# Performance work log

Measured on AMD Instinct MI355X. Metric: run time of the kernel, lower is better.

## Reference

```python
import jax, jax.numpy as jnp
import numpy as np

DIM = 128
N_ITER = 8
L_SIZE = 80000
C_SIZE = 120000
N_EDGES = 480000


def _mlp(x, w1, b1, w2, b2):
    # 2-layer MLP with ReLU (satbench_n_mlp_layers=2, activation='relu')
    return jnp.maximum(x @ w1 + b1, 0.0) @ w2 + b2


def _layer_norm(x, g, b, eps=1e-5):
    mu = jnp.mean(x, axis=-1, keepdims=True)
    var = jnp.var(x, axis=-1, keepdims=True)
    return (x - mu) * jax.lax.rsqrt(var + eps) * g + b


def _ln_lstm_cell(x, h, c, wi, wh, g_ih, b_ih, g_hh, b_hh, g_c, b_c):
    # LayerNormBasicLSTMCell: LN on input/hidden gate pre-activations and on new cell state
    gates = _layer_norm(x @ wi, g_ih, b_ih) + _layer_norm(h @ wh, g_hh, b_hh)
    i, f, g, o = jnp.split(gates, 4, axis=1)
    new_c = jax.nn.sigmoid(f) * c + jax.nn.sigmoid(i) * jnp.tanh(g)
    new_h = jax.nn.sigmoid(o) * jnp.tanh(_layer_norm(new_c, g_c, b_c))
    return new_h, new_c


def setup_inputs() -> dict:
    key = jax.random.key(0)
    ks = jax.random.split(key, 24)
    d = DIM
    s1 = 1.0 / np.sqrt(d)
    s2 = 1.0 / np.sqrt(2 * d)
    inp = {
        'l_size': L_SIZE,
        'c_size': C_SIZE,
        'l_edge_index': jax.random.randint(ks[0], (N_EDGES,), 0, L_SIZE),
        'c_edge_index': jax.random.randint(ks[1], (N_EDGES,), 0, C_SIZE),
        'l_emb': jax.random.normal(ks[2], (L_SIZE, d), jnp.float32),
        'c_emb': jax.random.normal(ks[3], (C_SIZE, d), jnp.float32),
        # l2c message MLP
        'l2c_w1': jax.random.normal(ks[4], (d, d), jnp.float32) * s1,
        'l2c_b1': jnp.zeros((d,), jnp.float32),
        'l2c_w2': jax.random.normal(ks[5], (d, d), jnp.float32) * s1,
        'l2c_b2': jnp.zeros((d,), jnp.float32),
        # c2l message MLP
        'c2l_w1': jax.random.normal(ks[6], (d, d), jnp.float32) * s1,
        'c2l_b1': jnp.zeros((d,), jnp.float32),
        'c2l_w2': jax.random.normal(ks[7], (d, d), jnp.float32) * s1,
        'c2l_b2': jnp.zeros((d,), jnp.float32),
        # clause update LSTM (input=d)
        'cu_wi': jax.random.normal(ks[8], (d, 4 * d), jnp.float32) * s1,
        'cu_wh': jax.random.normal(ks[9], (d, 4 * d), jnp.float32) * s1,
        'cu_g_ih': jnp.ones((4 * d,), jnp.float32),
        'cu_b_ih': jnp.zeros((4 * d,), jnp.float32),
        'cu_g_hh': jnp.ones((4 * d,), jnp.float32),
        'cu_b_hh': jnp.zeros((4 * d,), jnp.float32),
        'cu_g_c': jnp.ones((d,), jnp.float32),
        'cu_b_c': jnp.zeros((d,), jnp.float32),
        # literal update LSTM (input=2*d)
        'lu_wi': jax.random.normal(ks[10], (2 * d, 4 * d), jnp.float32) * s2,
        'lu_wh': jax.random.normal(ks[11], (d, 4 * d), jnp.float32) * s1,
        'lu_g_ih': jnp.ones((4 * d,), jnp.float32),
        'lu_b_ih': jnp.zeros((4 * d,), jnp.float32),
        'lu_g_hh': jnp.ones((4 * d,), jnp.float32),
        'lu_b_hh': jnp.zeros((4 * d,), jnp.float32),
        'lu_g_c': jnp.ones((d,), jnp.float32),
        'lu_b_c': jnp.zeros((d,), jnp.float32),
    }
    return inp


def reference(l_size, c_size, l_edge_index, c_edge_index, l_emb, c_emb,
              l2c_w1, l2c_b1, l2c_w2, l2c_b2,
              c2l_w1, c2l_b1, c2l_w2, c2l_b2,
              cu_wi, cu_wh, cu_g_ih, cu_b_ih, cu_g_hh, cu_b_hh, cu_g_c, cu_b_c,
              lu_wi, lu_wh, lu_g_ih, lu_b_ih, lu_g_hh, lu_b_hh, lu_g_c, lu_b_c):
    d = l_emb.shape[1]
    l_state = jnp.zeros((l_size, d), l_emb.dtype)
    c_state = jnp.zeros((c_size, d), c_emb.dtype)
    l_embs = [l_emb]
    c_embs = [c_emb]
    for _ in range(N_ITER):
        # literal -> clause
        l_msg_feat = _mlp(l_emb, l2c_w1, l2c_b1, l2c_w2, l2c_b2)
        l2c_msg = l_msg_feat[l_edge_index]                             # [E, d] gather
        l2c_aggr = jax.ops.segment_sum(l2c_msg, c_edge_index, num_segments=c_size)
        c_emb, c_state = _ln_lstm_cell(l2c_aggr, c_emb, c_state,
                                       cu_wi, cu_wh, cu_g_ih, cu_b_ih,
                                       cu_g_hh, cu_b_hh, cu_g_c, cu_b_c)
        c_embs.append(c_emb)
        # clause -> literal
        c_msg_feat = _mlp(c_emb, c2l_w1, c2l_b1, c2l_w2, c2l_b2)
        c2l_msg = c_msg_feat[c_edge_index]
        c2l_aggr = jax.ops.segment_sum(c2l_msg, l_edge_index, num_segments=l_size)
        # flip pos/neg literal embeddings (l2l message)
        pl, ul = jnp.split(l_emb.reshape(l_size // 2, 2 * d), 2, axis=1)
        l2l_msg = jnp.concatenate([ul, pl], axis=1).reshape(l_size, d)
        l_emb, l_state = _ln_lstm_cell(jnp.concatenate([c2l_aggr, l2l_msg], axis=1),
                                       l_emb, l_state,
                                       lu_wi, lu_wh, lu_g_ih, lu_b_ih,
                                       lu_g_hh, lu_b_hh, lu_g_c, lu_b_c)
        l_embs.append(l_emb)
    return jnp.stack(l_embs), jnp.stack(c_embs)
```

## Files before the change

### kernel.cpp

```cpp
#include <hip/hip_runtime.h>
#include <hip/hip_bf16.h>

#define L_SIZE 80000
#define C_SIZE 120000
#define N_EDGES 480000
#define DIM 128
#define GDIM 512
#define N_ITER 8

typedef __attribute__((ext_vector_type(8))) short short8;
typedef __attribute__((ext_vector_type(4))) float f32x4;

__device__ __forceinline__ ushort f2bf(float f) {
    uint u = __float_as_uint(f);
    u = u + 0x7FFFu + ((u >> 16) & 1u);
    return (ushort)(u >> 16);
}
__device__ __forceinline__ float bf2f(ushort h) {
    return __uint_as_float(((uint)h) << 16);
}
__device__ __forceinline__ float sigmf(float x) { return 1.f / (1.f + __expf(-x)); }
__device__ __forceinline__ float tanh_f(float x) {
    float e = __expf(2.f * x);
    return 1.f - 2.f / (e + 1.f);
}
__device__ __forceinline__ f32x4 fzero4() {
    f32x4 v; v[0] = v[1] = v[2] = v[3] = 0.f; return v;
}

__global__ __launch_bounds__(256) void count_kernel(
    const int* __restrict__ dst, int* __restrict__ counts)
{
    int i = blockIdx.x * 256 + threadIdx.x;
    atomicAdd(&counts[dst[i]], 1);
}

__global__ __launch_bounds__(1024) void scan_kernel(
    const int* __restrict__ counts, int* __restrict__ offsets, int n)
{
    __shared__ int psum[1024];
    const int tid = threadIdx.x;
    const int chunk = (n + 1023) / 1024;
    int lo = tid * chunk, hi = lo + chunk; if (hi > n) hi = n;
    int s = 0;
    for (int i = lo; i < hi; ++i) s += counts[i];
    psum[tid] = s;
    __syncthreads();
    for (int off = 1; off < 1024; off <<= 1) {
        int v = (tid >= off) ? psum[tid - off] : 0;
        __syncthreads();
        psum[tid] += v;
        __syncthreads();
    }
    int run = tid ? psum[tid - 1] : 0;
    for (int i = lo; i < hi; ++i) { offsets[i] = run; run += counts[i]; }
    if (tid == 1023) offsets[n] = run;
}

__global__ __launch_bounds__(256) void fill_kernel(
    const int* __restrict__ src, const int* __restrict__ dst,
    int* __restrict__ cursor, int* __restrict__ srclist)
{
    int i = blockIdx.x * 256 + threadIdx.x;
    int d = dst[i];
    int pos = atomicAdd(&cursor[d], 1);
    srclist[pos] = src[i];
}

__global__ __launch_bounds__(256) void aggregate_kernel(
    const float* __restrict__ msg, const int* __restrict__ offsets,
    const int* __restrict__ srclist, float* __restrict__ aggr, int nrows)
{
    int row = blockIdx.x * 8 + (threadIdx.x >> 5);
    if (row >= nrows) return;
    int d4 = (threadIdx.x & 31) << 2;
    int s = offsets[row], e = offsets[row + 1];
    float4 acc = {0.f, 0.f, 0.f, 0.f};
    for (int p = s; p < e; ++p) {
        int sr = srclist[p];
        float4 v = *(const float4*)(msg + (size_t)sr * DIM + d4);
        acc.x += v.x; acc.y += v.y; acc.z += v.z; acc.w += v.w;
    }
    *(float4*)(aggr + (size_t)row * DIM + d4) = acc;
}

__device__ __forceinline__ void stageA2(const float* __restrict__ src, int rowBase,
                                        int rowXor, ushort* dst, int tid, int nrows)
{
    const int planeB = nrows * 256;
    for (int idx = tid * 8; idx < nrows * 128; idx += 512 * 8) {
        int r = idx >> 7, k8 = idx & 127;
        const float* p = src + (size_t)((rowBase + r) ^ rowXor) * DIM + k8;
        float4 v0 = *(const float4*)p;
        float4 v1 = *(const float4*)(p + 4);
        float f[8] = {v0.x, v0.y, v0.z, v0.w, v1.x, v1.y, v1.z, v1.w};
        short8 hi, lo;
        #pragma unroll
        for (int j = 0; j < 8; ++j) {
            ushort h = f2bf(f[j]);
            hi[j] = (short)h;
            lo[j] = (short)f2bf(f[j] - bf2f(h));
        }
        int boff = r * 256 + ((k8 * 2) ^ ((r & 7) << 4));
        *(short8*)((char*)dst + boff) = hi;
        *(short8*)((char*)dst + planeB + boff) = lo;
    }
}

__device__ __forceinline__ short8 readA(const ushort* As, int mi, int k0, int lane)
{
    int r = mi * 16 + (lane & 15);
    int kb = (k0 * 2 + ((lane >> 4) << 4)) ^ ((r & 7) << 4);
    return *(const short8*)((const char*)As + r * 256 + kb);
}

__device__ __forceinline__ short8 readB(const ushort* P, int ks, int NC, int cc,
                                        int laneOff)
{
    return *(const short8*)((const char*)P + (((size_t)(ks * NC + cc)) << 10) + laneOff);
}

__global__ __launch_bounds__(256) void pack_w2(const float* __restrict__ W,
                                               ushort* __restrict__ Ph,
                                               ushort* __restrict__ Pl, int K, int N)
{
    int NC = N / 16;
    int total = K * N;
    for (int o = blockIdx.x * 256 + threadIdx.x; o < total; o += gridDim.x * 256) {
        int j = o & 7, hi = (o >> 3) & 3, c = (o >> 5) & 15;
        int rest = o >> 9;
        int cc = rest % NC, ks = rest / NC;
        int row = ks * 32 + hi * 8 + j, col = cc * 16 + c;
        float v = W[(size_t)row * N + col];
        ushort h = f2bf(v);
        Ph[o] = h;
        Pl[o] = f2bf(v - bf2f(h));
    }
}

#define MFMA3(acc, ah, al, bh, bl)                                              \
    acc = __builtin_amdgcn_mfma_f32_16x16x32_bf16(ah, bh, acc, 0, 0, 0);        \
    acc = __builtin_amdgcn_mfma_f32_16x16x32_bf16(ah, bl, acc, 0, 0, 0);        \
    acc = __builtin_amdgcn_mfma_f32_16x16x32_bf16(al, bh, acc, 0, 0, 0);

__global__ __launch_bounds__(512) void mlp_kernel(
    const float* __restrict__ A,
    const ushort* __restrict__ w1Ph, const ushort* __restrict__ w1Pl,
    const float* __restrict__ b1,
    const ushort* __restrict__ w2Ph, const ushort* __restrict__ w2Pl,
    const float* __restrict__ b2,
    float* __restrict__ msg)
{
    __shared__ __align__(16) ushort AsIn[2 * 64 * 128];
    __shared__ __align__(16) ushort AsHid[2 * 64 * 128];
    const int tid = threadIdx.x;
    const int wv = tid >> 6, lane = tid & 63;
    const int cl = lane & 15, hi = lane >> 4;
    const int rowBase = blockIdx.x * 64;
    const int laneOff = (cl * 4 + hi) * 16;
    const int col = wv * 16 + cl;

    stageA2(A, rowBase, 0, AsIn, tid, 64);
    float b1c = b1[col], b2c = b2[col];
    __syncthreads();

    f32x4 acc[4];
    #pragma unroll
    for (int mi = 0; mi < 4; ++mi) acc[mi] = fzero4();
    #pragma unroll
    for (int ks = 0; ks < 4; ++ks) {
        short8 bh = readB(w1Ph, ks, 8, wv, laneOff);
        short8 bl = readB(w1Pl, ks, 8, wv, laneOff);
        #pragma unroll
        for (int mi = 0; mi < 4; ++mi) {
            short8 ah = readA(AsIn, mi, ks * 32, lane);
            short8 al = readA(AsIn + 64 * 128, mi, ks * 32, lane);
            MFMA3(acc[mi], ah, al, bh, bl);
        }
    }
    #pragma unroll
    for (int mi = 0; mi < 4; ++mi)
        #pragma unroll
        for (int q = 0; q < 4; ++q) {
            int row = mi * 16 + hi * 4 + q;
            float v = fmaxf(acc[mi][q] + b1c, 0.f);
            ushort h = f2bf(v);
            int boff = row * 256 + ((2 * col) ^ ((row & 7) << 4));
            *(ushort*)((char*)AsHid + boff) = h;
            *(ushort*)((char*)AsHid + 64 * 256 + boff) = f2bf(v - bf2f(h));
        }
    __syncthreads();

    f32x4 acc2[4];
    #pragma unroll
    for (int mi = 0; mi < 4; ++mi) acc2[mi] = fzero4();
    #pragma unroll
    for (int ks = 0; ks < 4; ++ks) {
        short8 bh = readB(w2Ph, ks, 8, wv, laneOff);
        short8 bl = readB(w2Pl, ks, 8, wv, laneOff);
        #pragma unroll
        for (int mi = 0; mi < 4; ++mi) {
            short8 ah = readA(AsHid, mi, ks * 32, lane);
            short8 al = readA(AsHid + 64 * 128, mi, ks * 32, lane);
            MFMA3(acc2[mi], ah, al, bh, bl);
        }
    }
    #pragma unroll
    for (int mi = 0; mi < 4; ++mi)
        #pragma unroll
        for (int q = 0; q < 4; ++q) {
            int row = mi * 16 + hi * 4 + q;
            msg[(size_t)(rowBase + row) * DIM + col] = acc2[mi][q] + b2c;
        }
}

template<int KX>
__global__ __launch_bounds__(512) void lstm_kernel(
    const float* __restrict__ X0, const float* __restrict__ X1, int xor1,
    const float* __restrict__ Hsrc,
    const ushort* __restrict__ wiPh, const ushort* __restrict__ wiPl,
    const ushort* __restrict__ whPh, const ushort* __restrict__ whPl,
    const float* __restrict__ g_ih, const float* __restrict__ b_ih,
    const float* __restrict__ g_hh, const float* __restrict__ b_hh,
    const float* __restrict__ g_c,  const float* __restrict__ b_c,
    float* __restrict__ c_state, float* __restrict__ h_out)
{
    __shared__ __align__(16) ushort AsX0[2 * 32 * 128];
    __shared__ __align__(16) ushort AsX1[KX == 8 ? 2 * 32 * 128 : 8];
    __shared__ __align__(16) ushort AsH [2 * 32 * 128];
    __shared__ float red4[32][8][4];
    __shared__ float lnst[32][4];
    __shared__ float red2[32][8][2];
    __shared__ float lnc[32][2];

    const int tid = threadIdx.x;
    const int wv = tid >> 6, lane = tid & 63;
    const int cl = lane & 15, hi = lane >> 4;
    const int rowBase = blockIdx.x * 32;
    const int laneOff = (cl * 4 + hi) * 16;
    const int d = wv * 16 + cl;

    stageA2(X0, rowBase, 0, AsX0, tid, 32);
    if (KX == 8) stageA2(X1, rowBase, xor1, AsX1, tid, 32);
    stageA2(Hsrc, rowBase, 0, AsH, tid, 32);

    float gih[4], bih[4], ghh[4], bhh[4];
    #pragma unroll
    for (int jb = 0; jb < 4; ++jb) {
        int col = jb * 128 + d;
        gih[jb] = g_ih[col]; bih[jb] = b_ih[col];
        ghh[jb] = g_hh[col]; bhh[jb] = b_hh[col];
    }
    const float gcv = g_c[d], bcv = b_c[d];

    __syncthreads();

    f32x4 xacc[2][4], hacc[2][4];
    #pragma unroll
    for (int mi = 0; mi < 2; ++mi)
        #pragma unroll
        for (int jb = 0; jb < 4; ++jb) { xacc[mi][jb] = fzero4(); hacc[mi][jb] = fzero4(); }

    #pragma unroll
    for (int ks = 0; ks < KX; ++ks) {
        const ushort* AX = (KX == 8 && ks >= 4) ? AsX1 : AsX0;
        int k0 = (ks & 3) * 32;
        short8 axh0 = readA(AX, 0, k0, lane);
        short8 axl0 = readA(AX + 32 * 128, 0, k0, lane);
        short8 axh1 = readA(AX, 1, k0, lane);
        short8 axl1 = readA(AX + 32 * 128, 1, k0, lane);
        #pragma unroll
        for (int jb = 0; jb < 4; ++jb) {
            short8 bh = readB(wiPh, ks, 32, jb * 8 + wv, laneOff);
            short8 bl = readB(wiPl, ks, 32, jb * 8 + wv, laneOff);
            MFMA3(xacc[0][jb], axh0, axl0, bh, bl);
            MFMA3(xacc[1][jb], axh1, axl1, bh, bl);
        }
        if (ks < 4) {
            short8 ahh0 = readA(AsH, 0, k0, lane);
            short8 ahl0 = readA(AsH + 32 * 128, 0, k0, lane);
            short8 ahh1 = readA(AsH, 1, k0, lane);
            short8 ahl1 = readA(AsH + 32 * 128, 1, k0, lane);
            #pragma unroll
            for (int jb = 0; jb < 4; ++jb) {
                short8 bh = readB(whPh, ks, 32, jb * 8 + wv, laneOff);
                short8 bl = readB(whPl, ks, 32, jb * 8 + wv, laneOff);
                MFMA3(hacc[0][jb], ahh0, ahl0, bh, bl);
                MFMA3(hacc[1][jb], ahh1, ahl1, bh, bl);
            }
        }
    }

    #pragma unroll
    for (int mi = 0; mi < 2; ++mi)
        #pragma unroll
        for (int q = 0; q < 4; ++q) {
            float px = 0.f, pqx = 0.f, ph = 0.f, pqh = 0.f;
            #pragma unroll
            for (int jb = 0; jb < 4; ++jb) {
                float v = xacc[mi][jb][q]; px += v; pqx += v * v;
                float u = hacc[mi][jb][q]; ph += u; pqh += u * u;
            }
            #pragma unroll
            for (int m = 1; m < 16; m <<= 1) {
                px += __shfl_xor(px, m); pqx += __shfl_xor(pqx, m);
                ph += __shfl_xor(ph, m); pqh += __shfl_xor(pqh, m);
            }
            if (cl == 0) {
                int row = mi * 16 + hi * 4 + q;
                red4[row][wv][0] = px; red4[row][wv][1] = pqx;
                red4[row][wv][2] = ph; red4[row][wv][3] = pqh;
            }
        }
    __syncthreads();
    if (tid < 32) {
        float sx = 0.f, qx = 0.f, sh = 0.f, qh = 0.f;
        for (int ww = 0; ww < 8; ++ww) {
            sx += red4[tid][ww][0]; qx += red4[tid][ww][1];
            sh += red4[tid][ww][2]; qh += red4[tid][ww][3];
        }
        const float inv = 1.f / 512.f;
        float mux = sx * inv, muh = sh * inv;
        lnst[tid][0] = mux; lnst[tid][1] = rsqrtf(qx * inv - mux * mux + 1e-5f);
        lnst[tid][2] = muh; lnst[tid][3] = rsqrtf(qh * inv - muh * muh + 1e-5f);
    }
    __syncthreads();

    float cn[2][4], og[2][4];
    #pragma unroll
    for (int mi = 0; mi < 2; ++mi)
        #pragma unroll
        for (int q = 0; q < 4; ++q) {
            int row = mi * 16 + hi * 4 + q;
            float mux = lnst[row][0], rx = lnst[row][1];
            float muh = lnst[row][2], rh = lnst[row][3];
            float g4[4];
            #pragma unroll
            for (int jb = 0; jb < 4; ++jb)
                g4[jb] = (xacc[mi][jb][q] - mux) * rx * gih[jb] + bih[jb]
                       + (hacc[mi][jb][q] - muh) * rh * ghh[jb] + bhh[jb];
            float cp = c_state[(size_t)(rowBase + row) * DIM + d];
            float cv = sigmf(g4[1]) * cp + sigmf(g4[0]) * tanh_f(g4[2]);
            cn[mi][q] = cv; og[mi][q] = g4[3];
            float sc = cv, qc = cv * cv;
            #pragma unroll
            for (int m = 1; m < 16; m <<= 1) {
                sc += __shfl_xor(sc, m); qc += __shfl_xor(qc, m);
            }
            if (cl == 0) { red2[row][wv][0] = sc; red2[row][wv][1] = qc; }
        }
    __syncthreads();
    if (tid < 32) {
        float sc = 0.f, qc = 0.f;
        for (int ww = 0; ww < 8; ++ww) { sc += red2[tid][ww][0]; qc += red2[tid][ww][1]; }
        const float inv = 1.f / 128.f;
        float mu = sc * inv;
        lnc[tid][0] = mu; lnc[tid][1] = rsqrtf(qc * inv - mu * mu + 1e-5f);
    }
    __syncthreads();

    #pragma unroll
    for (int mi = 0; mi < 2; ++mi)
        #pragma unroll
        for (int q = 0; q < 4; ++q) {
            int row = mi * 16 + hi * 4 + q;
            size_t go = (size_t)(rowBase + row) * DIM + d;
            float cv = cn[mi][q];
            float hv = sigmf(og[mi][q]) *
                       tanh_f((cv - lnc[row][0]) * lnc[row][1] * gcv + bcv);
            c_state[go] = cv;
            h_out[go] = hv;
        }
}

extern "C" void kernel_launch(void* const* d_in, const int* in_sizes, int n_in,
                              void* d_out, int out_size, void* d_ws, size_t ws_size,
                              hipStream_t stream)
{
    const int*   l_edge  = (const int*)d_in[2];
    const int*   c_edge  = (const int*)d_in[3];
    const float* l_emb0  = (const float*)d_in[4];
    const float* c_emb0  = (const float*)d_in[5];
    const float* l2c_w1  = (const float*)d_in[6];
    const float* l2c_b1  = (const float*)d_in[7];
    const float* l2c_w2  = (const float*)d_in[8];
    const float* l2c_b2  = (const float*)d_in[9];
    const float* c2l_w1  = (const float*)d_in[10];
    const float* c2l_b1  = (const float*)d_in[11];
    const float* c2l_w2  = (const float*)d_in[12];
    const float* c2l_b2  = (const float*)d_in[13];
    const float* cu_wi   = (const float*)d_in[14];
    const float* cu_wh   = (const float*)d_in[15];
    const float* cu_g_ih = (const float*)d_in[16];
    const float* cu_b_ih = (const float*)d_in[17];
    const float* cu_g_hh = (const float*)d_in[18];
    const float* cu_b_hh = (const float*)d_in[19];
    const float* cu_g_c  = (const float*)d_in[20];
    const float* cu_b_c  = (const float*)d_in[21];
    const float* lu_wi   = (const float*)d_in[22];
    const float* lu_wh   = (const float*)d_in[23];
    const float* lu_g_ih = (const float*)d_in[24];
    const float* lu_b_ih = (const float*)d_in[25];
    const float* lu_g_hh = (const float*)d_in[26];
    const float* lu_b_hh = (const float*)d_in[27];
    const float* lu_g_c  = (const float*)d_in[28];
    const float* lu_b_c  = (const float*)d_in[29];

    float* out = (float*)d_out;
    float* l_slab = out;
    float* c_slab = out + (size_t)9 * L_SIZE * DIM;

    char* wp = (char*)d_ws;
    float*  l_state = (float*)wp;  wp += (size_t)L_SIZE * DIM * 4;
    float*  c_state = (float*)wp;  wp += (size_t)C_SIZE * DIM * 4;
    float*  aggr    = (float*)wp;  wp += (size_t)C_SIZE * DIM * 4;
    float*  msg     = (float*)wp;  wp += (size_t)C_SIZE * DIM * 4;
    int* c_off     = (int*)wp; wp += (C_SIZE + 1) * 4;
    int* l_off     = (int*)wp; wp += (L_SIZE + 1) * 4;
    int* cnt       = (int*)wp; wp += C_SIZE * 4;
    int* cursor    = (int*)wp; wp += C_SIZE * 4;
    int* c_srclist = (int*)wp; wp += N_EDGES * 4;
    int* l_srclist = (int*)wp; wp += N_EDGES * 4;
    ushort* l2c_w1Ph = (ushort*)wp; wp += 128 * 128 * 2;
    ushort* l2c_w1Pl = (ushort*)wp; wp += 128 * 128 * 2;
    ushort* l2c_w2Ph = (ushort*)wp; wp += 128 * 128 * 2;
    ushort* l2c_w2Pl = (ushort*)wp; wp += 128 * 128 * 2;
    ushort* c2l_w1Ph = (ushort*)wp; wp += 128 * 128 * 2;
    ushort* c2l_w1Pl = (ushort*)wp; wp += 128 * 128 * 2;
    ushort* c2l_w2Ph = (ushort*)wp; wp += 128 * 128 * 2;
    ushort* c2l_w2Pl = (ushort*)wp; wp += 128 * 128 * 2;
    ushort* cu_wiPh  = (ushort*)wp; wp += 128 * 512 * 2;
    ushort* cu_wiPl  = (ushort*)wp; wp += 128 * 512 * 2;
    ushort* cu_whPh  = (ushort*)wp; wp += 128 * 512 * 2;
    ushort* cu_whPl  = (ushort*)wp; wp += 128 * 512 * 2;
    ushort* lu_wiPh  = (ushort*)wp; wp += 256 * 512 * 2;
    ushort* lu_wiPl  = (ushort*)wp; wp += 256 * 512 * 2;
    ushort* lu_whPh  = (ushort*)wp; wp += 128 * 512 * 2;
    ushort* lu_whPl  = (ushort*)wp; wp += 128 * 512 * 2;

    const int eb = N_EDGES / 256;

    hipMemsetAsync(cnt, 0, C_SIZE * 4, stream);
    count_kernel<<<eb, 256, 0, stream>>>(c_edge, cnt);
    scan_kernel<<<1, 1024, 0, stream>>>(cnt, c_off, C_SIZE);
    hipMemcpyAsync(cursor, c_off, C_SIZE * 4, hipMemcpyDeviceToDevice, stream);
    fill_kernel<<<eb, 256, 0, stream>>>(l_edge, c_edge, cursor, c_srclist);
    hipMemsetAsync(cnt, 0, L_SIZE * 4, stream);
    count_kernel<<<eb, 256, 0, stream>>>(l_edge, cnt);
    scan_kernel<<<1, 1024, 0, stream>>>(cnt, l_off, L_SIZE);
    hipMemcpyAsync(cursor, l_off, L_SIZE * 4, hipMemcpyDeviceToDevice, stream);
    fill_kernel<<<eb, 256, 0, stream>>>(c_edge, l_edge, cursor, l_srclist);

    pack_w2<<<64, 256, 0, stream>>>(l2c_w1, l2c_w1Ph, l2c_w1Pl, 128, 128);
    pack_w2<<<64, 256, 0, stream>>>(l2c_w2, l2c_w2Ph, l2c_w2Pl, 128, 128);
    pack_w2<<<64, 256, 0, stream>>>(c2l_w1, c2l_w1Ph, c2l_w1Pl, 128, 128);
    pack_w2<<<64, 256, 0, stream>>>(c2l_w2, c2l_w2Ph, c2l_w2Pl, 128, 128);
    pack_w2<<<256, 256, 0, stream>>>(cu_wi, cu_wiPh, cu_wiPl, 128, 512);
    pack_w2<<<256, 256, 0, stream>>>(cu_wh, cu_whPh, cu_whPl, 128, 512);
    pack_w2<<<512, 256, 0, stream>>>(lu_wi, lu_wiPh, lu_wiPl, 256, 512);
    pack_w2<<<256, 256, 0, stream>>>(lu_wh, lu_whPh, lu_whPl, 128, 512);

    hipMemcpyAsync(l_slab, l_emb0, (size_t)L_SIZE * DIM * sizeof(float),
                   hipMemcpyDeviceToDevice, stream);
    hipMemcpyAsync(c_slab, c_emb0, (size_t)C_SIZE * DIM * sizeof(float),
                   hipMemcpyDeviceToDevice, stream);
    hipMemsetAsync(l_state, 0, (size_t)L_SIZE * DIM * sizeof(float), stream);
    hipMemsetAsync(c_state, 0, (size_t)C_SIZE * DIM * sizeof(float), stream);

    for (int t = 0; t < N_ITER; ++t) {
        const float* le = l_slab + (size_t)t * L_SIZE * DIM;
        const float* ce = c_slab + (size_t)t * C_SIZE * DIM;
        float* le1 = l_slab + (size_t)(t + 1) * L_SIZE * DIM;
        float* ce1 = c_slab + (size_t)(t + 1) * C_SIZE * DIM;

        mlp_kernel<<<L_SIZE / 64, 512, 0, stream>>>(le, l2c_w1Ph, l2c_w1Pl, l2c_b1,
                                                    l2c_w2Ph, l2c_w2Pl, l2c_b2, msg);
        aggregate_kernel<<<C_SIZE / 8, 256, 0, stream>>>(msg, c_off, c_srclist,
                                                         aggr, C_SIZE);
        lstm_kernel<4><<<C_SIZE / 32, 512, 0, stream>>>(
            aggr, nullptr, 0, ce, cu_wiPh, cu_wiPl, cu_whPh, cu_whPl,
            cu_g_ih, cu_b_ih, cu_g_hh, cu_b_hh, cu_g_c, cu_b_c,
            c_state, ce1);

        mlp_kernel<<<C_SIZE / 64, 512, 0, stream>>>(ce1, c2l_w1Ph, c2l_w1Pl, c2l_b1,
                                                    c2l_w2Ph, c2l_w2Pl, c2l_b2, msg);
        aggregate_kernel<<<L_SIZE / 8, 256, 0, stream>>>(msg, l_off, l_srclist,
                                                         aggr, L_SIZE);
        lstm_kernel<8><<<L_SIZE / 32, 512, 0, stream>>>(
            aggr, le, 1, le, lu_wiPh, lu_wiPl, lu_whPh, lu_whPl,
            lu_g_ih, lu_b_ih, lu_g_hh, lu_b_hh, lu_g_c, lu_b_c,
            l_state, le1);
    }
}
```

Before: 6.142 ms.

## Fuse iteration loop into persistent megakernel with grid barriers and fused aggregation

Replaces the 48 per-iteration kernel launches with one persistent kernel of 256 blocks. Each block loops over tiles of the MLP and LSTM phases, and the phases are separated by a software grid barrier built on an atomic counter. The segment-sum aggregation is folded into the LSTM staging, which drops the separate aggregate kernel and the fp32 aggr round-trip through memory. The cost is that only 256 blocks give lower parallelism and latency hiding, spin-wait barriers sit between phases, and forward progress depends on all 256 blocks being co-resident.

```diff
diff --git a/kernel.cpp b/kernel.cpp
--- a/kernel.cpp
+++ b/kernel.cpp
@@ -7,6 +7,8 @@
 #define DIM 128
 #define GDIM 512
 #define N_ITER 8
+#define NBLK 256
+#define NTHR 512
 
 typedef __attribute__((ext_vector_type(8))) short short8;
 typedef __attribute__((ext_vector_type(4))) float f32x4;
@@ -65,59 +67,6 @@
     int d = dst[i];
     int pos = atomicAdd(&cursor[d], 1);
     srclist[pos] = src[i];
-}
-
-__global__ __launch_bounds__(256) void aggregate_kernel(
-    const float* __restrict__ msg, const int* __restrict__ offsets,
-    const int* __restrict__ srclist, float* __restrict__ aggr, int nrows)
-{
-    int row = blockIdx.x * 8 + (threadIdx.x >> 5);
-    if (row >= nrows) return;
-    int d4 = (threadIdx.x & 31) << 2;
-    int s = offsets[row], e = offsets[row + 1];
-    float4 acc = {0.f, 0.f, 0.f, 0.f};
-    for (int p = s; p < e; ++p) {
-        int sr = srclist[p];
-        float4 v = *(const float4*)(msg + (size_t)sr * DIM + d4);
-        acc.x += v.x; acc.y += v.y; acc.z += v.z; acc.w += v.w;
-    }
-    *(float4*)(aggr + (size_t)row * DIM + d4) = acc;
-}
-
-__device__ __forceinline__ void stageA2(const float* __restrict__ src, int rowBase,
-                                        int rowXor, ushort* dst, int tid, int nrows)
-{
-    const int planeB = nrows * 256;
-    for (int idx = tid * 8; idx < nrows * 128; idx += 512 * 8) {
-        int r = idx >> 7, k8 = idx & 127;
-        const float* p = src + (size_t)((rowBase + r) ^ rowXor) * DIM + k8;
-        float4 v0 = *(const float4*)p;
-        float4 v1 = *(const float4*)(p + 4);
-        float f[8] = {v0.x, v0.y, v0.z, v0.w, v1.x, v1.y, v1.z, v1.w};
-        short8 hi, lo;
-        #pragma unroll
-        for (int j = 0; j < 8; ++j) {
-            ushort h = f2bf(f[j]);
-            hi[j] = (short)h;
-            lo[j] = (short)f2bf(f[j] - bf2f(h));
-        }
-        int boff = r * 256 + ((k8 * 2) ^ ((r & 7) << 4));
-        *(short8*)((char*)dst + boff) = hi;
-        *(short8*)((char*)dst + planeB + boff) = lo;
-    }
-}
-
-__device__ __forceinline__ short8 readA(const ushort* As, int mi, int k0, int lane)
-{
-    int r = mi * 16 + (lane & 15);
-    int kb = (k0 * 2 + ((lane >> 4) << 4)) ^ ((r & 7) << 4);
-    return *(const short8*)((const char*)As + r * 256 + kb);
-}
-
-__device__ __forceinline__ short8 readB(const ushort* P, int ks, int NC, int cc,
-                                        int laneOff)
-{
-    return *(const short8*)((const char*)P + (((size_t)(ks * NC + cc)) << 10) + laneOff);
 }
 
 __global__ __launch_bounds__(256) void pack_w2(const float* __restrict__ W,
@@ -138,29 +87,72 @@
     }
 }
 
+__device__ __forceinline__ void stageA2(const float* __restrict__ src, int rowBase,
+                                        int rowXor, ushort* dst, int tid, int nrows)
+{
+    const int planeB = nrows * 256;
+    for (int idx = tid * 8; idx < nrows * 128; idx += NTHR * 8) {
+        int r = idx >> 7, k8 = idx & 127;
+        const float* p = src + (size_t)((rowBase + r) ^ rowXor) * DIM + k8;
+        float4 v0 = *(const float4*)p;
+        float4 v1 = *(const float4*)(p + 4);
+        float f[8] = {v0.x, v0.y, v0.z, v0.w, v1.x, v1.y, v1.z, v1.w};
+        short8 hi8, lo8;
+        #pragma unroll
+        for (int j = 0; j < 8; ++j) {
+            ushort h = f2bf(f[j]);
+            hi8[j] = (short)h;
+            lo8[j] = (short)f2bf(f[j] - bf2f(h));
+        }
+        int boff = r * 256 + ((k8 * 2) ^ ((r & 7) << 4));
+        *(short8*)((char*)dst + boff) = hi8;
+        *(short8*)((char*)dst + planeB + boff) = lo8;
+    }
+}
+
+__device__ __forceinline__ short8 readA(const ushort* As, int mi, int k0, int lane)
+{
+    int r = mi * 16 + (lane & 15);
+    int kb = (k0 * 2 + ((lane >> 4) << 4)) ^ ((r & 7) << 4);
+    return *(const short8*)((const char*)As + r * 256 + kb);
+}
+
+__device__ __forceinline__ short8 readB(const ushort* P, int ks, int NC, int cc,
+                                        int laneOff)
+{
+    return *(const short8*)((const char*)P + (((size_t)(ks * NC + cc)) << 10) + laneOff);
+}
+
 #define MFMA3(acc, ah, al, bh, bl)                                              \
     acc = __builtin_amdgcn_mfma_f32_16x16x32_bf16(ah, bh, acc, 0, 0, 0);        \
     acc = __builtin_amdgcn_mfma_f32_16x16x32_bf16(ah, bl, acc, 0, 0, 0);        \
     acc = __builtin_amdgcn_mfma_f32_16x16x32_bf16(al, bh, acc, 0, 0, 0);
 
-__global__ __launch_bounds__(512) void mlp_kernel(
+__device__ __forceinline__ void grid_barrier(int* cnt, int target, int tid)
+{
+    __syncthreads();
+    if (tid == 0) {
+        __threadfence();
+        __hip_atomic_fetch_add(cnt, 1, __ATOMIC_ACQ_REL, __HIP_MEMORY_SCOPE_AGENT);
+        while (__hip_atomic_load(cnt, __ATOMIC_ACQUIRE, __HIP_MEMORY_SCOPE_AGENT) < target)
+            __builtin_amdgcn_s_sleep(2);
+        __threadfence();
+    }
+    __syncthreads();
+}
+
+__device__ __forceinline__ void mlp_block(
     const float* __restrict__ A,
     const ushort* __restrict__ w1Ph, const ushort* __restrict__ w1Pl,
     const float* __restrict__ b1,
     const ushort* __restrict__ w2Ph, const ushort* __restrict__ w2Pl,
     const float* __restrict__ b2,
-    float* __restrict__ msg)
-{
-    __shared__ __align__(16) ushort AsIn[2 * 64 * 128];
-    __shared__ __align__(16) ushort AsHid[2 * 64 * 128];
-    const int tid = threadIdx.x;
-    const int wv = tid >> 6, lane = tid & 63;
-    const int cl = lane & 15, hi = lane >> 4;
-    const int rowBase = blockIdx.x * 64;
-    const int laneOff = (cl * 4 + hi) * 16;
+    float* __restrict__ msg, int rowBase,
+    ushort* AsIn, ushort* AsHid,
+    int tid, int wv, int lane, int cl, int hi, int laneOff)
+{
+    stageA2(A, rowBase, 0, AsIn, tid, 64);
     const int col = wv * 16 + cl;
-
-    stageA2(A, rowBase, 0, AsIn, tid, 64);
     float b1c = b1[col], b2c = b2[col];
     __syncthreads();
 
@@ -212,38 +204,53 @@
             int row = mi * 16 + hi * 4 + q;
             msg[(size_t)(rowBase + row) * DIM + col] = acc2[mi][q] + b2c;
         }
+    __syncthreads();
 }
 
 template<int KX>
-__global__ __launch_bounds__(512) void lstm_kernel(
-    const float* __restrict__ X0, const float* __restrict__ X1, int xor1,
-    const float* __restrict__ Hsrc,
+__device__ __forceinline__ void lstm_block(
+    const float* __restrict__ msg, const int* __restrict__ offs,
+    const int* __restrict__ srcl,
+    const float* __restrict__ X1src, const float* __restrict__ Hsrc,
     const ushort* __restrict__ wiPh, const ushort* __restrict__ wiPl,
     const ushort* __restrict__ whPh, const ushort* __restrict__ whPl,
     const float* __restrict__ g_ih, const float* __restrict__ b_ih,
     const float* __restrict__ g_hh, const float* __restrict__ b_hh,
     const float* __restrict__ g_c,  const float* __restrict__ b_c,
-    float* __restrict__ c_state, float* __restrict__ h_out)
-{
-    __shared__ __align__(16) ushort AsX0[2 * 32 * 128];
-    __shared__ __align__(16) ushort AsX1[KX == 8 ? 2 * 32 * 128 : 8];
-    __shared__ __align__(16) ushort AsH [2 * 32 * 128];
-    __shared__ float red4[32][8][4];
-    __shared__ float lnst[32][4];
-    __shared__ float red2[32][8][2];
-    __shared__ float lnc[32][2];
-
-    const int tid = threadIdx.x;
-    const int wv = tid >> 6, lane = tid & 63;
-    const int cl = lane & 15, hi = lane >> 4;
-    const int rowBase = blockIdx.x * 32;
-    const int laneOff = (cl * 4 + hi) * 16;
+    float* __restrict__ c_state, float* __restrict__ h_out, int rowBase,
+    ushort* AsX0, ushort* AsX1, ushort* AsH,
+    float (*red4)[8][4], float (*lnst)[4], float (*red2)[8][2], float (*lnc)[2],
+    int tid, int wv, int lane, int cl, int hi, int laneOff)
+{
+    {
+        int r = tid >> 4;
+        int d8 = (tid & 15) << 3;
+        int row = rowBase + r;
+        int s = offs[row], e = offs[row + 1];
+        float a0=0,a1=0,a2=0,a3=0,a4=0,a5=0,a6=0,a7=0;
+        for (int p = s; p < e; ++p) {
+            const float* mp = msg + (size_t)srcl[p] * DIM + d8;
+            float4 v0 = *(const float4*)mp;
+            float4 v1 = *(const float4*)(mp + 4);
+            a0 += v0.x; a1 += v0.y; a2 += v0.z; a3 += v0.w;
+            a4 += v1.x; a5 += v1.y; a6 += v1.z; a7 += v1.w;
+        }
+        float f[8] = {a0,a1,a2,a3,a4,a5,a6,a7};
+        short8 hi8, lo8;
+        #pragma unroll
+        for (int j = 0; j < 8; ++j) {
+            ushort h = f2bf(f[j]);
+            hi8[j] = (short)h;
+            lo8[j] = (short)f2bf(f[j] - bf2f(h));
+        }
+        int boff = r * 256 + ((d8 * 2) ^ ((r & 7) << 4));
+        *(short8*)((char*)AsX0 + boff) = hi8;
+        *(short8*)((char*)AsX0 + 32 * 256 + boff) = lo8;
+    }
+    stageA2(Hsrc, rowBase, 0, AsH, tid, 32);
+    if (KX == 8) stageA2(X1src, rowBase, 1, AsX1, tid, 32);
+
     const int d = wv * 16 + cl;
-
-    stageA2(X0, rowBase, 0, AsX0, tid, 32);
-    if (KX == 8) stageA2(X1, rowBase, xor1, AsX1, tid, 32);
-    stageA2(Hsrc, rowBase, 0, AsH, tid, 32);
-
     float gih[4], bih[4], ghh[4], bhh[4];
     #pragma unroll
     for (int jb = 0; jb < 4; ++jb) {
@@ -252,7 +259,6 @@
         ghh[jb] = g_hh[col]; bhh[jb] = b_hh[col];
     }
     const float gcv = g_c[d], bcv = b_c[d];
-
     __syncthreads();
 
     f32x4 xacc[2][4], hacc[2][4];
@@ -371,6 +377,84 @@
             c_state[go] = cv;
             h_out[go] = hv;
         }
+    __syncthreads();
+}
+
+__global__ __launch_bounds__(NTHR, 2) void mega_kernel(
+    float* __restrict__ l_slab, float* __restrict__ c_slab,
+    float* __restrict__ l_state, float* __restrict__ c_state,
+    float* __restrict__ msg,
+    const int* __restrict__ c_off, const int* __restrict__ c_srclist,
+    const int* __restrict__ l_off, const int* __restrict__ l_srclist,
+    const ushort* l2c_w1Ph, const ushort* l2c_w1Pl, const float* l2c_b1,
+    const ushort* l2c_w2Ph, const ushort* l2c_w2Pl, const float* l2c_b2,
+    const ushort* c2l_w1Ph, const ushort* c2l_w1Pl, const float* c2l_b1,
+    const ushort* c2l_w2Ph, const ushort* c2l_w2Pl, const float* c2l_b2,
+    const ushort* cu_wiPh, const ushort* cu_wiPl,
+    const ushort* cu_whPh, const ushort* cu_whPl,
+    const float* cu_g_ih, const float* cu_b_ih,
+    const float* cu_g_hh, const float* cu_b_hh,
+    const float* cu_g_c,  const float* cu_b_c,
+    const ushort* lu_wiPh, const ushort* lu_wiPl,
+    const ushort* lu_whPh, const ushort* lu_whPl,
+    const float* lu_g_ih, const float* lu_b_ih,
+    const float* lu_g_hh, const float* lu_b_hh,
+    const float* lu_g_c,  const float* lu_b_c,
+    int* __restrict__ barCnt)
+{
+    __shared__ __align__(16) union ShU {
+        struct { ushort in[2 * 64 * 128]; ushort hid[2 * 64 * 128]; } m;
+        struct {
+            ushort x0[2 * 32 * 128];
+            ushort x1[2 * 32 * 128];
+            ushort h [2 * 32 * 128];
+            float red4[32][8][4];
+            float lnst[32][4];
+            float red2[32][8][2];
+            float lnc[32][2];
+        } s;
+    } sh;
+
+    const int tid = threadIdx.x;
+    const int wv = tid >> 6, lane = tid & 63;
+    const int cl = lane & 15, hi = lane >> 4;
+    const int laneOff = (cl * 4 + hi) * 16;
+    int bar = 0;
+
+    for (int t = 0; t < N_ITER; ++t) {
+        const float* le = l_slab + (size_t)t * L_SIZE * DIM;
+        const float* ce = c_slab + (size_t)t * C_SIZE * DIM;
+        float* le1 = l_slab + (size_t)(t + 1) * L_SIZE * DIM;
+        float* ce1 = c_slab + (size_t)(t + 1) * C_SIZE * DIM;
+
+        for (int tb = blockIdx.x; tb < L_SIZE / 64; tb += NBLK)
+            mlp_block(le, l2c_w1Ph, l2c_w1Pl, l2c_b1, l2c_w2Ph, l2c_w2Pl, l2c_b2,
+                      msg, tb * 64, sh.m.in, sh.m.hid, tid, wv, lane, cl, hi, laneOff);
+        grid_barrier(barCnt, (++bar) * NBLK, tid);
+
+        for (int tb = blockIdx.x; tb < C_SIZE / 32; tb += NBLK)
+            lstm_block<4>(msg, c_off, c_srclist, nullptr, ce,
+                          cu_wiPh, cu_wiPl, cu_whPh, cu_whPl,
+                          cu_g_ih, cu_b_ih, cu_g_hh, cu_b_hh, cu_g_c, cu_b_c,
+                          c_state, ce1, tb * 32,
+                          sh.s.x0, sh.s.x1, sh.s.h, sh.s.red4, sh.s.lnst,
+                          sh.s.red2, sh.s.lnc, tid, wv, lane, cl, hi, laneOff);
+        grid_barrier(barCnt, (++bar) * NBLK, tid);
+
+        for (int tb = blockIdx.x; tb < C_SIZE / 64; tb += NBLK)
+            mlp_block(ce1, c2l_w1Ph, c2l_w1Pl, c2l_b1, c2l_w2Ph, c2l_w2Pl, c2l_b2,
+                      msg, tb * 64, sh.m.in, sh.m.hid, tid, wv, lane, cl, hi, laneOff);
+        grid_barrier(barCnt, (++bar) * NBLK, tid);
+
+        for (int tb = blockIdx.x; tb < L_SIZE / 32; tb += NBLK)
+            lstm_block<8>(msg, l_off, l_srclist, le, le,
+                          lu_wiPh, lu_wiPl, lu_whPh, lu_whPl,
+                          lu_g_ih, lu_b_ih, lu_g_hh, lu_b_hh, lu_g_c, lu_b_c,
+                          l_state, le1, tb * 32,
+                          sh.s.x0, sh.s.x1, sh.s.h, sh.s.red4, sh.s.lnst,
+                          sh.s.red2, sh.s.lnc, tid, wv, lane, cl, hi, laneOff);
+        grid_barrier(barCnt, (++bar) * NBLK, tid);
+    }
 }
 
 extern "C" void kernel_launch(void* const* d_in, const int* in_sizes, int n_in,
@@ -413,7 +497,6 @@
     char* wp = (char*)d_ws;
     float*  l_state = (float*)wp;  wp += (size_t)L_SIZE * DIM * 4;
     float*  c_state = (float*)wp;  wp += (size_t)C_SIZE * DIM * 4;
-    float*  aggr    = (float*)wp;  wp += (size_t)C_SIZE * DIM * 4;
     float*  msg     = (float*)wp;  wp += (size_t)C_SIZE * DIM * 4;
     int* c_off     = (int*)wp; wp += (C_SIZE + 1) * 4;
     int* l_off     = (int*)wp; wp += (L_SIZE + 1) * 4;
@@ -421,6 +504,7 @@
     int* cursor    = (int*)wp; wp += C_SIZE * 4;
     int* c_srclist = (int*)wp; wp += N_EDGES * 4;
     int* l_srclist = (int*)wp; wp += N_EDGES * 4;
+    int* barCnt    = (int*)wp; wp += 64;
     ushort* l2c_w1Ph = (ushort*)wp; wp += 128 * 128 * 2;
     ushort* l2c_w1Pl = (ushort*)wp; wp += 128 * 128 * 2;
     ushort* l2c_w2Ph = (ushort*)wp; wp += 128 * 128 * 2;
@@ -466,29 +550,16 @@
                    hipMemcpyDeviceToDevice, stream);
     hipMemsetAsync(l_state, 0, (size_t)L_SIZE * DIM * sizeof(float), stream);
     hipMemsetAsync(c_state, 0, (size_t)C_SIZE * DIM * sizeof(float), stream);
-
-    for (int t = 0; t < N_ITER; ++t) {
-        const float* le = l_slab + (size_t)t * L_SIZE * DIM;
-        const float* ce = c_slab + (size_t)t * C_SIZE * DIM;
-        float* le1 = l_slab + (size_t)(t + 1) * L_SIZE * DIM;
-        float* ce1 = c_slab + (size_t)(t + 1) * C_SIZE * DIM;
-
-        mlp_kernel<<<L_SIZE / 64, 512, 0, stream>>>(le, l2c_w1Ph, l2c_w1Pl, l2c_b1,
-                                                    l2c_w2Ph, l2c_w2Pl, l2c_b2, msg);
-        aggregate_kernel<<<C_SIZE / 8, 256, 0, stream>>>(msg, c_off, c_srclist,
-                                                         aggr, C_SIZE);
-        lstm_kernel<4><<<C_SIZE / 32, 512, 0, stream>>>(
-            aggr, nullptr, 0, ce, cu_wiPh, cu_wiPl, cu_whPh, cu_whPl,
-            cu_g_ih, cu_b_ih, cu_g_hh, cu_b_hh, cu_g_c, cu_b_c,
-            c_state, ce1);
-
-        mlp_kernel<<<C_SIZE / 64, 512, 0, stream>>>(ce1, c2l_w1Ph, c2l_w1Pl, c2l_b1,
-                                                    c2l_w2Ph, c2l_w2Pl, c2l_b2, msg);
-        aggregate_kernel<<<L_SIZE / 8, 256, 0, stream>>>(msg, l_off, l_srclist,
-                                                         aggr, L_SIZE);
-        lstm_kernel<8><<<L_SIZE / 32, 512, 0, stream>>>(
-            aggr, le, 1, le, lu_wiPh, lu_wiPl, lu_whPh, lu_whPl,
-            lu_g_ih, lu_b_ih, lu_g_hh, lu_b_hh, lu_g_c, lu_b_c,
-            l_state, le1);
-    }
-}
+    hipMemsetAsync(barCnt, 0, 64, stream);
+
+    mega_kernel<<<NBLK, NTHR, 0, stream>>>(
+        l_slab, c_slab, l_state, c_state, msg,
+        c_off, c_srclist, l_off, l_srclist,
+        l2c_w1Ph, l2c_w1Pl, l2c_b1, l2c_w2Ph, l2c_w2Pl, l2c_b2,
+        c2l_w1Ph, c2l_w1Pl, c2l_b1, c2l_w2Ph, c2l_w2Pl, c2l_b2,
+        cu_wiPh, cu_wiPl, cu_whPh, cu_whPl,
+        cu_g_ih, cu_b_ih, cu_g_hh, cu_b_hh, cu_g_c, cu_b_c,
+        lu_wiPh, lu_wiPl, lu_whPh, lu_whPl,
+        lu_g_ih, lu_b_ih, lu_g_hh, lu_b_hh, lu_g_c, lu_b_c,
+        barCnt);
+}
```

Result: slower. 13.15 ms (+114.1%).

## Fuse CSR segment-sum aggregation into LSTM kernel staging and pad reductions

Applied to the files above, without the earlier changes.

Removes the separate aggregate kernel and the aggr buffer. Each LSTM block now gathers and sums incoming messages for its own 32 rows directly into shared memory as split bf16 hi/lo, which saves a global write and read of the aggregate and a kernel launch per half-iteration. It also adds a minimum-blocks hint of 4 to the launch bounds of the MLP and LSTM kernels, and pads the shared reduction arrays to avoid bank conflicts. The risks are that the gather latency now sits inside the MFMA kernel with one thread per 8 columns, and that the occupancy hint may force register spills.

```diff
diff --git a/kernel.cpp b/kernel.cpp
--- a/kernel.cpp
+++ b/kernel.cpp
@@ -65,59 +65,6 @@
     int d = dst[i];
     int pos = atomicAdd(&cursor[d], 1);
     srclist[pos] = src[i];
-}
-
-__global__ __launch_bounds__(256) void aggregate_kernel(
-    const float* __restrict__ msg, const int* __restrict__ offsets,
-    const int* __restrict__ srclist, float* __restrict__ aggr, int nrows)
-{
-    int row = blockIdx.x * 8 + (threadIdx.x >> 5);
-    if (row >= nrows) return;
-    int d4 = (threadIdx.x & 31) << 2;
-    int s = offsets[row], e = offsets[row + 1];
-    float4 acc = {0.f, 0.f, 0.f, 0.f};
-    for (int p = s; p < e; ++p) {
-        int sr = srclist[p];
-        float4 v = *(const float4*)(msg + (size_t)sr * DIM + d4);
-        acc.x += v.x; acc.y += v.y; acc.z += v.z; acc.w += v.w;
-    }
-    *(float4*)(aggr + (size_t)row * DIM + d4) = acc;
-}
-
-__device__ __forceinline__ void stageA2(const float* __restrict__ src, int rowBase,
-                                        int rowXor, ushort* dst, int tid, int nrows)
-{
-    const int planeB = nrows * 256;
-    for (int idx = tid * 8; idx < nrows * 128; idx += 512 * 8) {
-        int r = idx >> 7, k8 = idx & 127;
-        const float* p = src + (size_t)((rowBase + r) ^ rowXor) * DIM + k8;
-        float4 v0 = *(const float4*)p;
-        float4 v1 = *(const float4*)(p + 4);
-        float f[8] = {v0.x, v0.y, v0.z, v0.w, v1.x, v1.y, v1.z, v1.w};
-        short8 hi, lo;
-        #pragma unroll
-        for (int j = 0; j < 8; ++j) {
-            ushort h = f2bf(f[j]);
-            hi[j] = (short)h;
-            lo[j] = (short)f2bf(f[j] - bf2f(h));
-        }
-        int boff = r * 256 + ((k8 * 2) ^ ((r & 7) << 4));
-        *(short8*)((char*)dst + boff) = hi;
-        *(short8*)((char*)dst + planeB + boff) = lo;
-    }
-}
-
-__device__ __forceinline__ short8 readA(const ushort* As, int mi, int k0, int lane)
-{
-    int r = mi * 16 + (lane & 15);
-    int kb = (k0 * 2 + ((lane >> 4) << 4)) ^ ((r & 7) << 4);
-    return *(const short8*)((const char*)As + r * 256 + kb);
-}
-
-__device__ __forceinline__ short8 readB(const ushort* P, int ks, int NC, int cc,
-                                        int laneOff)
-{
-    return *(const short8*)((const char*)P + (((size_t)(ks * NC + cc)) << 10) + laneOff);
 }
 
 __global__ __launch_bounds__(256) void pack_w2(const float* __restrict__ W,
@@ -138,12 +85,48 @@
     }
 }
 
+__device__ __forceinline__ void stageA2(const float* __restrict__ src, int rowBase,
+                                        int rowXor, ushort* dst, int tid, int nrows)
+{
+    const int planeB = nrows * 256;
+    for (int idx = tid * 8; idx < nrows * 128; idx += 512 * 8) {
+        int r = idx >> 7, k8 = idx & 127;
+        const float* p = src + (size_t)((rowBase + r) ^ rowXor) * DIM + k8;
+        float4 v0 = *(const float4*)p;
+        float4 v1 = *(const float4*)(p + 4);
+        float f[8] = {v0.x, v0.y, v0.z, v0.w, v1.x, v1.y, v1.z, v1.w};
+        short8 hi8, lo8;
+        #pragma unroll
+        for (int j = 0; j < 8; ++j) {
+            ushort h = f2bf(f[j]);
+            hi8[j] = (short)h;
+            lo8[j] = (short)f2bf(f[j] - bf2f(h));
+        }
+        int boff = r * 256 + ((k8 * 2) ^ ((r & 7) << 4));
+        *(short8*)((char*)dst + boff) = hi8;
+        *(short8*)((char*)dst + planeB + boff) = lo8;
+    }
+}
+
+__device__ __forceinline__ short8 readA(const ushort* As, int mi, int k0, int lane)
+{
+    int r = mi * 16 + (lane & 15);
+    int kb = (k0 * 2 + ((lane >> 4) << 4)) ^ ((r & 7) << 4);
+    return *(const short8*)((const char*)As + r * 256 + kb);
+}
+
+__device__ __forceinline__ short8 readB(const ushort* P, int ks, int NC, int cc,
+                                        int laneOff)
+{
+    return *(const short8*)((const char*)P + (((size_t)(ks * NC + cc)) << 10) + laneOff);
+}
+
 #define MFMA3(acc, ah, al, bh, bl)                                              \
     acc = __builtin_amdgcn_mfma_f32_16x16x32_bf16(ah, bh, acc, 0, 0, 0);        \
     acc = __builtin_amdgcn_mfma_f32_16x16x32_bf16(ah, bl, acc, 0, 0, 0);        \
     acc = __builtin_amdgcn_mfma_f32_16x16x32_bf16(al, bh, acc, 0, 0, 0);
 
-__global__ __launch_bounds__(512) void mlp_kernel(
+__global__ __launch_bounds__(512, 4) void mlp_kernel(
     const float* __restrict__ A,
     const ushort* __restrict__ w1Ph, const ushort* __restrict__ w1Pl,
     const float* __restrict__ b1,
@@ -215,9 +198,10 @@
 }
 
 template<int KX>
-__global__ __launch_bounds__(512) void lstm_kernel(
-    const float* __restrict__ X0, const float* __restrict__ X1, int xor1,
-    const float* __restrict__ Hsrc,
+__global__ __launch_bounds__(512, 4) void lstm_kernel(
+    const float* __restrict__ msg, const int* __restrict__ offs,
+    const int* __restrict__ srcl,
+    const float* __restrict__ X1src, const float* __restrict__ Hsrc,
     const ushort* __restrict__ wiPh, const ushort* __restrict__ wiPl,
     const ushort* __restrict__ whPh, const ushort* __restrict__ whPl,
     const float* __restrict__ g_ih, const float* __restrict__ b_ih,
@@ -228,10 +212,10 @@
     __shared__ __align__(16) ushort AsX0[2 * 32 * 128];
     __shared__ __align__(16) ushort AsX1[KX == 8 ? 2 * 32 * 128 : 8];
     __shared__ __align__(16) ushort AsH [2 * 32 * 128];
-    __shared__ float red4[32][8][4];
-    __shared__ float lnst[32][4];
-    __shared__ float red2[32][8][2];
-    __shared__ float lnc[32][2];
+    __shared__ float red4f[32 * 33];
+    __shared__ float lnstf[32 * 4];
+    __shared__ float red2f[32 * 17];
+    __shared__ float lncf[32 * 2];
 
     const int tid = threadIdx.x;
     const int wv = tid >> 6, lane = tid & 63;
@@ -240,9 +224,33 @@
     const int laneOff = (cl * 4 + hi) * 16;
     const int d = wv * 16 + cl;
 
-    stageA2(X0, rowBase, 0, AsX0, tid, 32);
-    if (KX == 8) stageA2(X1, rowBase, xor1, AsX1, tid, 32);
+    {
+        int r = tid >> 4;
+        int d8 = (tid & 15) << 3;
+        int row = rowBase + r;
+        int s = offs[row], e = offs[row + 1];
+        float a0=0,a1=0,a2=0,a3=0,a4=0,a5=0,a6=0,a7=0;
+        for (int p = s; p < e; ++p) {
+            const float* mp = msg + (size_t)srcl[p] * DIM + d8;
+            float4 v0 = *(const float4*)mp;
+            float4 v1 = *(const float4*)(mp + 4);
+            a0 += v0.x; a1 += v0.y; a2 += v0.z; a3 += v0.w;
+            a4 += v1.x; a5 += v1.y; a6 += v1.z; a7 += v1.w;
+        }
+        float f[8] = {a0,a1,a2,a3,a4,a5,a6,a7};
+        short8 hi8, lo8;
+        #pragma unroll
+        for (int j = 0; j < 8; ++j) {
+            ushort h = f2bf(f[j]);
+            hi8[j] = (short)h;
+            lo8[j] = (short)f2bf(f[j] - bf2f(h));
+        }
+        int boff = r * 256 + ((d8 * 2) ^ ((r & 7) << 4));
+        *(short8*)((char*)AsX0 + boff) = hi8;
+        *(short8*)((char*)AsX0 + 32 * 256 + boff) = lo8;
+    }
     stageA2(Hsrc, rowBase, 0, AsH, tid, 32);
+    if (KX == 8) stageA2(X1src, rowBase, 1, AsX1, tid, 32);
 
     float gih[4], bih[4], ghh[4], bhh[4];
     #pragma unroll
@@ -252,7 +260,6 @@
         ghh[jb] = g_hh[col]; bhh[jb] = b_hh[col];
     }
     const float gcv = g_c[d], bcv = b_c[d];
-
     __syncthreads();
 
     f32x4 xacc[2][4], hacc[2][4];
@@ -308,21 +315,24 @@
             }
             if (cl == 0) {
                 int row = mi * 16 + hi * 4 + q;
-                red4[row][wv][0] = px; red4[row][wv][1] = pqx;
-                red4[row][wv][2] = ph; red4[row][wv][3] = pqh;
+                float* rp = red4f + row * 33 + wv * 4;
+                rp[0] = px; rp[1] = pqx; rp[2] = ph; rp[3] = pqh;
             }
         }
     __syncthreads();
     if (tid < 32) {
         float sx = 0.f, qx = 0.f, sh = 0.f, qh = 0.f;
+        const float* rp = red4f + tid * 33;
         for (int ww = 0; ww < 8; ++ww) {
-            sx += red4[tid][ww][0]; qx += red4[tid][ww][1];
-            sh += red4[tid][ww][2]; qh += red4[tid][ww][3];
+            sx += rp[ww * 4 + 0]; qx += rp[ww * 4 + 1];
+            sh += rp[ww * 4 + 2]; qh += rp[ww * 4 + 3];
         }
         const float inv = 1.f / 512.f;
         float mux = sx * inv, muh = sh * inv;
-        lnst[tid][0] = mux; lnst[tid][1] = rsqrtf(qx * inv - mux * mux + 1e-5f);
-        lnst[tid][2] = muh; lnst[tid][3] = rsqrtf(qh * inv - muh * muh + 1e-5f);
+        lnstf[tid * 4 + 0] = mux;
+        lnstf[tid * 4 + 1] = rsqrtf(qx * inv - mux * mux + 1e-5f);
+        lnstf[tid * 4 + 2] = muh;
+        lnstf[tid * 4 + 3] = rsqrtf(qh * inv - muh * muh + 1e-5f);
     }
     __syncthreads();
 
@@ -332,8 +342,8 @@
         #pragma unroll
         for (int q = 0; q < 4; ++q) {
             int row = mi * 16 + hi * 4 + q;
-            float mux = lnst[row][0], rx = lnst[row][1];
-            float muh = lnst[row][2], rh = lnst[row][3];
+            float mux = lnstf[row * 4 + 0], rx = lnstf[row * 4 + 1];
+            float muh = lnstf[row * 4 + 2], rh = lnstf[row * 4 + 3];
             float g4[4];
             #pragma unroll
             for (int jb = 0; jb < 4; ++jb)
@@ -347,15 +357,20 @@
             for (int m = 1; m < 16; m <<= 1) {
                 sc += __shfl_xor(sc, m); qc += __shfl_xor(qc, m);
             }
-            if (cl == 0) { red2[row][wv][0] = sc; red2[row][wv][1] = qc; }
+            if (cl == 0) {
+                float* rp = red2f + row * 17 + wv * 2;
+                rp[0] = sc; rp[1] = qc;
+            }
         }
     __syncthreads();
     if (tid < 32) {
         float sc = 0.f, qc = 0.f;
-        for (int ww = 0; ww < 8; ++ww) { sc += red2[tid][ww][0]; qc += red2[tid][ww][1]; }
+        const float* rp = red2f + tid * 17;
+        for (int ww = 0; ww < 8; ++ww) { sc += rp[ww * 2]; qc += rp[ww * 2 + 1]; }
         const float inv = 1.f / 128.f;
         float mu = sc * inv;
-        lnc[tid][0] = mu; lnc[tid][1] = rsqrtf(qc * inv - mu * mu + 1e-5f);
+        lncf[tid * 2 + 0] = mu;
+        lncf[tid * 2 + 1] = rsqrtf(qc * inv - mu * mu + 1e-5f);
     }
     __syncthreads();
 
@@ -367,7 +382,7 @@
             size_t go = (size_t)(rowBase + row) * DIM + d;
             float cv = cn[mi][q];
             float hv = sigmf(og[mi][q]) *
-                       tanh_f((cv - lnc[row][0]) * lnc[row][1] * gcv + bcv);
+                       tanh_f((cv - lncf[row * 2]) * lncf[row * 2 + 1] * gcv + bcv);
             c_state[go] = cv;
             h_out[go] = hv;
         }
@@ -413,7 +428,6 @@
     char* wp = (char*)d_ws;
     float*  l_state = (float*)wp;  wp += (size_t)L_SIZE * DIM * 4;
     float*  c_state = (float*)wp;  wp += (size_t)C_SIZE * DIM * 4;
-    float*  aggr    = (float*)wp;  wp += (size_t)C_SIZE * DIM * 4;
     float*  msg     = (float*)wp;  wp += (size_t)C_SIZE * DIM * 4;
     int* c_off     = (int*)wp; wp += (C_SIZE + 1) * 4;
     int* l_off     = (int*)wp; wp += (L_SIZE + 1) * 4;
@@ -475,19 +489,17 @@
 
         mlp_kernel<<<L_SIZE / 64, 512, 0, stream>>>(le, l2c_w1Ph, l2c_w1Pl, l2c_b1,
                                                     l2c_w2Ph, l2c_w2Pl, l2c_b2, msg);
-        aggregate_kernel<<<C_SIZE / 8, 256, 0, stream>>>(msg, c_off, c_srclist,
-                                                         aggr, C_SIZE);
         lstm_kernel<4><<<C_SIZE / 32, 512, 0, stream>>>(
-            aggr, nullptr, 0, ce, cu_wiPh, cu_wiPl, cu_whPh, cu_whPl,
+            msg, c_off, c_srclist, nullptr, ce,
+            cu_wiPh, cu_wiPl, cu_whPh, cu_whPl,
             cu_g_ih, cu_b_ih, cu_g_hh, cu_b_hh, cu_g_c, cu_b_c,
             c_state, ce1);
 
         mlp_kernel<<<C_SIZE / 64, 512, 0, stream>>>(ce1, c2l_w1Ph, c2l_w1Pl, c2l_b1,
                                                     c2l_w2Ph, c2l_w2Pl, c2l_b2, msg);
-        aggregate_kernel<<<L_SIZE / 8, 256, 0, stream>>>(msg, l_off, l_srclist,
-                                                         aggr, L_SIZE);
         lstm_kernel<8><<<L_SIZE / 32, 512, 0, stream>>>(
-            aggr, le, 1, le, lu_wiPh, lu_wiPl, lu_whPh, lu_whPl,
+            msg, l_off, l_srclist, le, le,
+            lu_wiPh, lu_wiPl, lu_whPh, lu_whPl,
             lu_g_ih, lu_b_ih, lu_g_hh, lu_b_hh, lu_g_c, lu_b_c,
             l_state, le1);
     }
```

After: 5.792 ms. -5.7%, faster.
